# Performance work log

Measured on AMD Instinct MI355X. Metric: run time of the kernel, lower is better.

Reference implementation:

```python
import jax, jax.numpy as jnp
import numpy as np

B, QLEN, MLEN, E, H, DH = 2, 1024, 1024, 1024, 16, 64
KLEN = QLEN + MLEN
LN_EPS = 1e-3  # keras LayerNormalization default epsilon


def layer_norm(x, gamma, beta):
    mu = jnp.mean(x, axis=-1, keepdims=True)
    var = jnp.mean(jnp.square(x - mu), axis=-1, keepdims=True)
    return (x - mu) * jax.lax.rsqrt(var + LN_EPS) * gamma + beta


def rel_shift(x):
    # x: [B, H, q, k] -> standard Transformer-XL relative shift
    b, h, q, k = x.shape
    x = jnp.pad(x, ((0, 0), (0, 0), (0, 0), (1, 0)))
    x = x.reshape(b, h, k + 1, q)[:, :, 1:, :]
    return x.reshape(b, h, q, k)


def setup_inputs() -> dict:
    key = jax.random.key(0)
    ks = jax.random.split(key, 12)
    s = 0.02
    inp = {
        "w": jax.random.normal(ks[0], (B, QLEN, E), jnp.float32),
        "r": jax.random.normal(ks[1], (1, KLEN, E), jnp.float32),
        "member": jax.random.normal(ks[2], (B, MLEN, E), jnp.float32),
        # causal mask over concatenated keys: 1 = masked
        "attn_mask": (jnp.arange(KLEN)[None, :] > (jnp.arange(QLEN)[:, None] + MLEN)).astype(jnp.float32),
        "Wq": jax.random.normal(ks[3], (E, H * DH), jnp.float32) * s,
        "Wk": jax.random.normal(ks[4], (E, H * DH), jnp.float32) * s,
        "Wv": jax.random.normal(ks[5], (E, H * DH), jnp.float32) * s,
        "Wr": jax.random.normal(ks[6], (E, H * DH), jnp.float32) * s,
        "Wo": jax.random.normal(ks[7], (H * DH, E), jnp.float32) * s,
        "r_w_bias": jnp.zeros((H, DH), jnp.float32),
        "r_r_bias": jnp.zeros((H, DH), jnp.float32),
        "ln1_g": jnp.ones((E,), jnp.float32),
        "ln1_b": jnp.zeros((E,), jnp.float32),
        "W1": jax.random.normal(ks[8], (E, 4 * E), jnp.float32) * s,
        "W2": jax.random.normal(ks[9], (4 * E, E), jnp.float32) * s,
        "ln2_g": jnp.ones((E,), jnp.float32),
        "ln2_b": jnp.zeros((E,), jnp.float32),
    }
    return inp


def reference(w, r, member, attn_mask, Wq, Wk, Wv, Wr, Wo, r_w_bias, r_r_bias,
              ln1_g, ln1_b, W1, W2, ln2_g, ln2_b):
    b, qlen, e = w.shape
    h, dh = r_w_bias.shape
    cat = jnp.concatenate([member, w], axis=1)          # [B, klen, E]
    q = (cat @ Wq)[:, -qlen:]                           # [B, q, H*DH]
    k = cat @ Wk                                        # [B, klen, H*DH]
    v = cat @ Wv
    rp = (r @ Wr)[0]                                    # [klen, H*DH] (shared over batch)
    qh = q.reshape(b, qlen, h, dh)
    kh = k.reshape(b, -1, h, dh)
    vh = v.reshape(b, -1, h, dh)
    rh = rp.reshape(-1, h, dh)
    AC = jnp.einsum('bqhd,bkhd->bhqk', qh + r_w_bias, kh)
    BD = jnp.einsum('bqhd,khd->bhqk', qh + r_r_bias, rh)
    BD = rel_shift(BD)
    attn = (AC + BD) / jnp.sqrt(jnp.float32(e))         # note: scaled by sqrt(embed_size)
    m = attn_mask[None, None]                           # [1,1,q,klen]
    attn = attn * (1.0 - m) - 1e30 * m
    p = jax.nn.softmax(attn, axis=-1)
    o = jnp.einsum('bhqk,bkhd->bqhd', p, vh).reshape(b, qlen, h * dh)
    o = o @ Wo
    x = layer_norm(w + o, ln1_g, ln1_b)
    y = jax.nn.relu(x @ W1) @ W2
    return layer_norm(y + x, ln2_g, ln2_b)
```

## Files before the change

### kernel.cpp

```cpp
#include <hip/hip_runtime.h>
#include <hip/hip_bf16.h>
#include <stdint.h>

typedef __bf16 bf16x8 __attribute__((ext_vector_type(8)));
typedef float  f32x4  __attribute__((ext_vector_type(4)));

constexpr int BB   = 2;
constexpr int QL   = 1024;
constexpr int ML   = 1024;
constexpr int KL   = 2048;
constexpr int ED   = 1024;
constexpr int HH   = 16;
constexpr int FF   = 4096;
constexpr size_t MN = 2048u * 1024u;

__device__ __forceinline__ bf16x8 ld8(const __hip_bfloat16* p) {
    return *reinterpret_cast<const bf16x8*>(p);
}
__device__ __forceinline__ void st8(__hip_bfloat16* p, bf16x8 v) {
    *reinterpret_cast<bf16x8*>(p) = v;
}
__device__ __forceinline__ f32x4 mfma16(bf16x8 a, bf16x8 b, f32x4 c) {
    return __builtin_amdgcn_mfma_f32_16x16x32_bf16(a, b, c, 0, 0, 0);
}
__device__ __forceinline__ void async16(void* lds, const void* g) {
    __builtin_amdgcn_global_load_lds((__attribute__((address_space(1))) void*)g,
                                     (__attribute__((address_space(3))) void*)lds,
                                     16, 0, 0);
}

__global__ __launch_bounds__(256) void build_cat_r(const float* __restrict__ w,
                                                   const float* __restrict__ mem,
                                                   const float* __restrict__ r,
                                                   __hip_bfloat16* __restrict__ cat,
                                                   __hip_bfloat16* __restrict__ rbf) {
    const int bx = blockIdx.x;
    const float* src;
    __hip_bfloat16* dst;
    size_t g;
    if (bx < 2048) {
        size_t t = (size_t)bx * 256 + threadIdx.x;
        g = t * 8;
        int b   = (int)(g >> 21);
        int rem = (int)(g & ((1u << 21) - 1));
        int j = rem >> 10, e = rem & 1023;
        src = (j < ML) ? &mem[((size_t)b * ML + j) * ED + e]
                       : &w[((size_t)b * QL + (j - ML)) * ED + e];
        dst = &cat[g];
    } else {
        g = ((size_t)(bx - 2048) * 256 + threadIdx.x) * 8;
        src = &r[g];
        dst = &rbf[g];
    }
    float4 f0 = *(const float4*)src;
    float4 f1 = *(const float4*)(src + 4);
    union { bf16x8 v; __hip_bfloat16 h[8]; } u;
    u.h[0] = __float2bfloat16(f0.x); u.h[1] = __float2bfloat16(f0.y);
    u.h[2] = __float2bfloat16(f0.z); u.h[3] = __float2bfloat16(f0.w);
    u.h[4] = __float2bfloat16(f1.x); u.h[5] = __float2bfloat16(f1.y);
    u.h[6] = __float2bfloat16(f1.z); u.h[7] = __float2bfloat16(f1.w);
    st8(dst, u.v);
}

__global__ __launch_bounds__(256) void transpose_cast(const float* __restrict__ in,
                                                      __hip_bfloat16* __restrict__ out,
                                                      int K, int N) {
    __shared__ float tile[32][33];
    const int tx = threadIdx.x & 31, ty = threadIdx.x >> 5;
    const int n0 = blockIdx.x * 32, k0 = blockIdx.y * 32;
#pragma unroll
    for (int i = 0; i < 4; ++i)
        tile[ty + i * 8][tx] = in[(size_t)(k0 + ty + i * 8) * N + n0 + tx];
    __syncthreads();
#pragma unroll
    for (int i = 0; i < 4; ++i)
        out[(size_t)(n0 + ty + i * 8) * K + k0 + tx] = __float2bfloat16(tile[tx][ty + i * 8]);
}

__global__ __launch_bounds__(256) void tc5(const float* __restrict__ s0, const float* __restrict__ s1,
                                           const float* __restrict__ s2, const float* __restrict__ s3,
                                           const float* __restrict__ s4,
                                           __hip_bfloat16* __restrict__ wqkvT,
                                           __hip_bfloat16* __restrict__ wot) {
    __shared__ float tile[32][33];
    const int z = blockIdx.z;
    const float* in = (z == 0) ? s0 : (z == 1) ? s1 : (z == 2) ? s2 : (z == 3) ? s3 : s4;
    __hip_bfloat16* out = (z == 4) ? wot : wqkvT + (size_t)z * 1024 * 1024;
    const int tx = threadIdx.x & 31, ty = threadIdx.x >> 5;
    const int n0 = blockIdx.x * 32, k0 = blockIdx.y * 32;
#pragma unroll
    for (int i = 0; i < 4; ++i)
        tile[ty + i * 8][tx] = in[(size_t)(k0 + ty + i * 8) * 1024 + n0 + tx];
    __syncthreads();
#pragma unroll
    for (int i = 0; i < 4; ++i)
        out[(size_t)(n0 + ty + i * 8) * 1024 + k0 + tx] = __float2bfloat16(tile[tx][ty + i * 8]);
}

__global__ __launch_bounds__(256) void transpose_v(const __hip_bfloat16* __restrict__ v,
                                                   __hip_bfloat16* __restrict__ vt) {
    __shared__ __hip_bfloat16 tile[32][33];
    const int tx = threadIdx.x & 31, ty = threadIdx.x >> 5;
    const int s = blockIdx.z, b = s >> 4, h = s & 15;
    const int j0 = blockIdx.x * 32, d0 = blockIdx.y * 32;
#pragma unroll
    for (int i = 0; i < 4; ++i)
        tile[ty + i * 8][tx] =
            v[((size_t)b * KL + j0 + ty + i * 8) * 1024 + h * 64 + d0 + tx];
    __syncthreads();
#pragma unroll
    for (int i = 0; i < 4; ++i)
        vt[((size_t)s * 64 + d0 + ty + i * 8) * KL + j0 + tx] = tile[tx][ty + i * 8];
}

template <int EPI, bool SK>
__global__ __launch_bounds__(256) void gemm_bt(const __hip_bfloat16* __restrict__ A,
                                               const __hip_bfloat16* __restrict__ Bt,
                                               void* __restrict__ Cv,
                                               int N, int kLen, int lda, int ldb) {
    __shared__ __align__(16) __hip_bfloat16 sA[128 * 32];
    __shared__ __align__(16) __hip_bfloat16 sB[128 * 32];
    const int tid = threadIdx.x;
    const int lane = tid & 63;
    const int l16 = lane & 15, quad = lane >> 4;
    const int wv = tid >> 6;
    const int wm = wv >> 1, wn = wv & 1;
    const int bm = blockIdx.y * 128, bn = blockIdx.x * 128;
    const int kOff = SK ? blockIdx.z * kLen : 0;
    const int c0 = tid, c1 = 256 + tid;
    const int r0 = c0 >> 2, o0 = (c0 & 3) * 8;
    const int r1 = c1 >> 2, o1 = (c1 & 3) * 8;
    f32x4 acc[4][4] = {};
    for (int k0 = 0; k0 < kLen; k0 += 32) {
        async16(&sA[c0 * 8], A + (size_t)(bm + r0) * lda + kOff + k0 + o0);
        async16(&sA[c1 * 8], A + (size_t)(bm + r1) * lda + kOff + k0 + o1);
        async16(&sB[c0 * 8], Bt + (size_t)(bn + r0) * ldb + kOff + k0 + o0);
        async16(&sB[c1 * 8], Bt + (size_t)(bn + r1) * ldb + kOff + k0 + o1);
        __syncthreads();
        bf16x8 af[4], bfr[4];
#pragma unroll
        for (int i = 0; i < 4; ++i)
            af[i] = ld8(&sA[(wm * 64 + i * 16 + l16) * 32 + quad * 8]);
#pragma unroll
        for (int j = 0; j < 4; ++j)
            bfr[j] = ld8(&sB[(wn * 64 + j * 16 + l16) * 32 + quad * 8]);
#pragma unroll
        for (int i = 0; i < 4; ++i)
#pragma unroll
            for (int j = 0; j < 4; ++j)
                acc[i][j] = mfma16(af[i], bfr[j], acc[i][j]);
        __syncthreads();
    }
#pragma unroll
    for (int i = 0; i < 4; ++i)
#pragma unroll
        for (int j = 0; j < 4; ++j)
#pragma unroll
            for (int rg = 0; rg < 4; ++rg) {
                size_t row = bm + wm * 64 + i * 16 + quad * 4 + rg;
                size_t col = bn + wn * 64 + j * 16 + l16;
                float v = acc[i][j][rg];
                if (EPI == 0) {
                    float* C = (float*)Cv + (SK ? (size_t)blockIdx.z * MN : 0);
                    C[row * N + col] = v;
                } else {
                    __hip_bfloat16* C = (__hip_bfloat16*)Cv;
                    C[row * N + col] = __float2bfloat16(fmaxf(v, 0.f));
                }
            }
}

__global__ __launch_bounds__(256) void gemm_qkvr(const __hip_bfloat16* __restrict__ cat,
                                                 const __hip_bfloat16* __restrict__ rbf,
                                                 const __hip_bfloat16* __restrict__ Bt,
                                                 __hip_bfloat16* __restrict__ qwb,
                                                 __hip_bfloat16* __restrict__ qrb,
                                                 __hip_bfloat16* __restrict__ kbuf,
                                                 __hip_bfloat16* __restrict__ vbuf,
                                                 __hip_bfloat16* __restrict__ rpb,
                                                 const float* __restrict__ rwb,
                                                 const float* __restrict__ rrb) {
    const int bm = blockIdx.y * 128, bn = blockIdx.x * 128;
    const int region = blockIdx.x >> 3;
    if (region == 0 && (bm & 2047) < 1024) return;
    if (region == 3 && bm >= 2048) return;
    const __hip_bfloat16* A = (region == 3) ? rbf : cat;
    __shared__ __align__(16) __hip_bfloat16 sA[128 * 32];
    __shared__ __align__(16) __hip_bfloat16 sB[128 * 32];
    const int tid = threadIdx.x;
    const int lane = tid & 63;
    const int l16 = lane & 15, quad = lane >> 4;
    const int wv = tid >> 6;
    const int wm = wv >> 1, wn = wv & 1;
    const int c0 = tid, c1 = 256 + tid;
    const int r0 = c0 >> 2, o0 = (c0 & 3) * 8;
    const int r1 = c1 >> 2, o1 = (c1 & 3) * 8;
    f32x4 acc[4][4] = {};
    for (int k0 = 0; k0 < 1024; k0 += 32) {
        async16(&sA[c0 * 8], A + (size_t)(bm + r0) * 1024 + k0 + o0);
        async16(&sA[c1 * 8], A + (size_t)(bm + r1) * 1024 + k0 + o1);
        async16(&sB[c0 * 8], Bt + (size_t)(bn + r0) * 1024 + k0 + o0);
        async16(&sB[c1 * 8], Bt + (size_t)(bn + r1) * 1024 + k0 + o1);
        __syncthreads();
        bf16x8 af[4], bfr[4];
#pragma unroll
        for (int i = 0; i < 4; ++i)
            af[i] = ld8(&sA[(wm * 64 + i * 16 + l16) * 32 + quad * 8]);
#pragma unroll
        for (int j = 0; j < 4; ++j)
            bfr[j] = ld8(&sB[(wn * 64 + j * 16 + l16) * 32 + quad * 8]);
#pragma unroll
        for (int i = 0; i < 4; ++i)
#pragma unroll
            for (int j = 0; j < 4; ++j)
                acc[i][j] = mfma16(af[i], bfr[j], acc[i][j]);
        __syncthreads();
    }
#pragma unroll
    for (int j = 0; j < 4; ++j) {
        const int col = bn + wn * 64 + j * 16 + l16;
        float bw = 0.f, br = 0.f;
        if (region == 0) { bw = rwb[col]; br = rrb[col]; }
#pragma unroll
        for (int i = 0; i < 4; ++i)
#pragma unroll
            for (int rg = 0; rg < 4; ++rg) {
                const int row = bm + wm * 64 + i * 16 + quad * 4 + rg;
                const int bb = row >> 11, jr = row & 2047;
                float v = acc[i][j][rg];
                if (region == 0) {
                    size_t o = ((size_t)(bb * 1024 + (jr - 1024))) * 1024 + col;
                    qwb[o] = __float2bfloat16(v + bw);
                    qrb[o] = __float2bfloat16(v + br);
                } else if (region == 1) {
                    kbuf[((size_t)(bb * 2048 + jr)) * 1024 + (col - 1024)] = __float2bfloat16(v);
                } else if (region == 2) {
                    vbuf[((size_t)(bb * 2048 + jr)) * 1024 + (col - 2048)] = __float2bfloat16(v);
                } else {
                    rpb[(size_t)row * 1024 + (col - 3072)] = __float2bfloat16(v);
                }
            }
    }
}

__global__ __launch_bounds__(64, 3) void flash_attn3(
        const __hip_bfloat16* __restrict__ qw, const __hip_bfloat16* __restrict__ qr,
        const __hip_bfloat16* __restrict__ kbuf, const __hip_bfloat16* __restrict__ vtb,
        const __hip_bfloat16* __restrict__ rpb,
        float* __restrict__ Opart, float* __restrict__ lpart) {
    __shared__ __align__(16) __hip_bfloat16 spb[32][76];
    const int lane = threadIdx.x;
    const int l16 = lane & 15, quad = lane >> 4;
    const int qi = blockIdx.x >> 1, chunk = blockIdx.x & 1;
    const int h = blockIdx.y, b = blockIdx.z;
    const int i0 = qi * 32;

    bf16x8 qaw[2][2], qar[2][2];
#pragma unroll
    for (int g = 0; g < 2; ++g)
#pragma unroll
        for (int kf = 0; kf < 2; ++kf) {
            size_t qi_ = ((size_t)(b * QL + i0 + g * 16 + l16)) * 1024 + h * 64 + kf * 32 + quad * 8;
            qaw[g][kf] = ld8(&qw[qi_]);
            qar[g][kf] = ld8(&qr[qi_]);
        }
    f32x4 oacc[2][4] = {};
    f32x4 lacc[2] = {};
    union { bf16x8 v; __hip_bfloat16 h8[8]; } ou;
#pragma unroll
    for (int j = 0; j < 8; ++j) ou.h8[j] = __float2bfloat16(l16 == 0 ? 1.f : 0.f);
    const bf16x8 onesf = ou.v;

    int srcIdx[4], selr[4];
#pragma unroll
    for (int r = 0; r < 4; ++r) {
        int s = l16 + 15 - (quad * 4 + r);
        selr[r] = s >> 4;
        srcIdx[r] = (quad * 16) | (s & 15);
    }
    const int T = (i0 + 1119) >> 6, Ta = T >> 1;
    const int t0 = chunk ? Ta : 0, t1 = chunk ? T : Ta;
    const __hip_bfloat16* kB = kbuf + (size_t)b * KL * 1024 + h * 64;
    const __hip_bfloat16* vB = vtb + ((size_t)(b * HH + h) * 64) * 2048;
    const __hip_bfloat16* rB = rpb + h * 64;

    for (int jt = t0; jt < t1; ++jt) {
        const int j0 = jt * 64;
        f32x4 sfr[2][4];
#pragma unroll
        for (int nt = 0; nt < 4; ++nt) {
            const __hip_bfloat16* kr = kB + (size_t)(j0 + nt * 16 + l16) * 1024 + quad * 8;
            bf16x8 b0 = ld8(kr);
            bf16x8 b1 = ld8(kr + 32);
#pragma unroll
            for (int g = 0; g < 2; ++g) {
                f32x4 z = {};
                z = mfma16(qaw[g][0], b0, z);
                z = mfma16(qaw[g][1], b1, z);
                sfr[g][nt] = z;
            }
        }
        f32x4 bd[2][5];
        const int ubase = j0 - i0 + 992;
#pragma unroll
        for (int s = 0; s < 6; ++s) {
            int row = ubase + s * 16 + l16;
            if (row > 2047) row = 2047;
            const __hip_bfloat16* rr = rB + (size_t)row * 1024 + quad * 8;
            bf16x8 f0 = ld8(rr);
            bf16x8 f1 = ld8(rr + 32);
            if (s >= 1) {
                f32x4 z = {};
                z = mfma16(qar[0][0], f0, z);
                z = mfma16(qar[0][1], f1, z);
                bd[0][s - 1] = z;
            }
            if (s <= 4) {
                f32x4 z = {};
                z = mfma16(qar[1][0], f0, z);
                z = mfma16(qar[1][1], f1, z);
                bd[1][s] = z;
            }
        }
#pragma unroll
        for (int g = 0; g < 2; ++g) {
            float pre[5][4];
#pragma unroll
            for (int t = 0; t < 5; ++t)
#pragma unroll
                for (int r = 0; r < 4; ++r)
                    pre[t][r] = __shfl(bd[g][t][r], srcIdx[r], 64);
#pragma unroll
            for (int nt = 0; nt < 4; ++nt)
#pragma unroll
                for (int r = 0; r < 4; ++r) {
                    float bdv = selr[r] ? pre[nt + 1][r] : pre[nt][r];
                    float sv = (sfr[g][nt][r] + bdv) * 0.03125f;
                    int ii = i0 + g * 16 + quad * 4 + r;
                    int jj = j0 + nt * 16 + l16;
                    float p = (jj <= ii + ML) ? __expf(sv) : 0.f;
                    spb[g * 16 + quad * 4 + r][nt * 16 + l16] = __float2bfloat16(p);
                }
        }
        bf16x8 pa[2][2];
#pragma unroll
        for (int g = 0; g < 2; ++g) {
            pa[g][0] = ld8(&spb[g * 16 + l16][quad * 8]);
            pa[g][1] = ld8(&spb[g * 16 + l16][32 + quad * 8]);
            lacc[g] = mfma16(pa[g][0], onesf, lacc[g]);
            lacc[g] = mfma16(pa[g][1], onesf, lacc[g]);
        }
#pragma unroll
        for (int dt = 0; dt < 4; ++dt) {
            const __hip_bfloat16* vr = vB + (size_t)(dt * 16 + l16) * 2048 + j0 + quad * 8;
            bf16x8 v0 = ld8(vr);
            bf16x8 v1 = ld8(vr + 32);
#pragma unroll
            for (int g = 0; g < 2; ++g) {
                oacc[g][dt] = mfma16(pa[g][0], v0, oacc[g][dt]);
                oacc[g][dt] = mfma16(pa[g][1], v1, oacc[g][dt]);
            }
        }
    }
    const size_t obase = ((size_t)((chunk * 2 + b) * HH + h)) * (1024 * 64);
#pragma unroll
    for (int g = 0; g < 2; ++g)
#pragma unroll
        for (int dt = 0; dt < 4; ++dt)
#pragma unroll
            for (int r = 0; r < 4; ++r) {
                int q = i0 + g * 16 + quad * 4 + r;
                Opart[obase + (size_t)q * 64 + dt * 16 + l16] = oacc[g][dt][r];
            }
    if (l16 == 0) {
        const size_t lbase = ((size_t)((chunk * 2 + b) * HH + h)) * 1024;
#pragma unroll
        for (int g = 0; g < 2; ++g)
#pragma unroll
            for (int r = 0; r < 4; ++r) {
                int q = i0 + g * 16 + quad * 4 + r;
                lpart[lbase + q] = lacc[g][r];
            }
    }
}

__global__ __launch_bounds__(256) void combine_attn(const float* __restrict__ Opart,
                                                    const float* __restrict__ lpart,
                                                    __hip_bfloat16* __restrict__ og) {
    size_t t = (size_t)blockIdx.x * 256 + threadIdx.x;
    size_t e4 = t * 4;
    int d  = (int)(e4 & 63);
    int q  = (int)((e4 >> 6) & 1023);
    int hh = (int)((e4 >> 16) & 15);
    int bb = (int)(e4 >> 20);
    size_t i0 = ((size_t)(bb * HH + hh) * 1024 + q) * 64 + d;
    const size_t CS = (size_t)2 * HH * 1024 * 64;
    float4 o0 = *(const float4*)&Opart[i0];
    float4 o1 = *(const float4*)&Opart[i0 + CS];
    float l0 = lpart[(size_t)(bb * HH + hh) * 1024 + q];
    float l1 = lpart[(size_t)(bb * HH + hh) * 1024 + q + 2 * HH * 1024];
    float inv = 1.f / (l0 + l1);
    union { __hip_bfloat16 h[4]; uint2 u; } o;
    o.h[0] = __float2bfloat16((o0.x + o1.x) * inv);
    o.h[1] = __float2bfloat16((o0.y + o1.y) * inv);
    o.h[2] = __float2bfloat16((o0.z + o1.z) * inv);
    o.h[3] = __float2bfloat16((o0.w + o1.w) * inv);
    *(uint2*)&og[((size_t)bb * 1024 + q) * 1024 + hh * 64 + d] = o.u;
}

template <int NP, bool WB>
__global__ __launch_bounds__(256) void add_ln_k(const float* __restrict__ res,
                                                const float* __restrict__ parts,
                                                const float* __restrict__ gam,
                                                const float* __restrict__ bet,
                                                float* __restrict__ of,
                                                __hip_bfloat16* __restrict__ ob) {
    const int tid = threadIdx.x;
    const size_t base = (size_t)blockIdx.x * ED;
    const int col = tid * 4;
    float4 va = *(const float4*)&res[base + col];
    float x0 = va.x, x1 = va.y, x2 = va.z, x3 = va.w;
#pragma unroll
    for (int z = 0; z < NP; ++z) {
        float4 p = *(const float4*)&parts[(size_t)z * MN + base + col];
        x0 += p.x; x1 += p.y; x2 += p.z; x3 += p.w;
    }
    float s1 = x0 + x1 + x2 + x3;
    float s2 = x0 * x0 + x1 * x1 + x2 * x2 + x3 * x3;
    for (int o = 32; o > 0; o >>= 1) {
        s1 += __shfl_down(s1, o, 64);
        s2 += __shfl_down(s2, o, 64);
    }
    __shared__ float p1[4], p2[4];
    if ((tid & 63) == 0) { p1[tid >> 6] = s1; p2[tid >> 6] = s2; }
    __syncthreads();
    float S1 = p1[0] + p1[1] + p1[2] + p1[3];
    float S2 = p2[0] + p2[1] + p2[2] + p2[3];
    float mu = S1 * (1.0f / ED);
    float var = S2 * (1.0f / ED) - mu * mu;
    float rs = rsqrtf(var + 1e-3f);
    float4 g4 = *(const float4*)&gam[col];
    float4 b4 = *(const float4*)&bet[col];
    float y0 = (x0 - mu) * rs * g4.x + b4.x;
    float y1 = (x1 - mu) * rs * g4.y + b4.y;
    float y2 = (x2 - mu) * rs * g4.z + b4.z;
    float y3 = (x3 - mu) * rs * g4.w + b4.w;
    *(float4*)&of[base + col] = make_float4(y0, y1, y2, y3);
    if (WB) {
        ob[base + col + 0] = __float2bfloat16(y0);
        ob[base + col + 1] = __float2bfloat16(y1);
        ob[base + col + 2] = __float2bfloat16(y2);
        ob[base + col + 3] = __float2bfloat16(y3);
    }
}

extern "C" void kernel_launch(void* const* d_in, const int* in_sizes, int n_in,
                              void* d_out, int out_size, void* d_ws, size_t ws_size,
                              hipStream_t stream) {
    const float* w   = (const float*)d_in[0];
    const float* r   = (const float*)d_in[1];
    const float* mem = (const float*)d_in[2];
    const float* Wq  = (const float*)d_in[4];
    const float* Wk  = (const float*)d_in[5];
    const float* Wv  = (const float*)d_in[6];
    const float* Wr  = (const float*)d_in[7];
    const float* Wo  = (const float*)d_in[8];
    const float* rwb = (const float*)d_in[9];
    const float* rrb = (const float*)d_in[10];
    const float* g1  = (const float*)d_in[11];
    const float* b1  = (const float*)d_in[12];
    const float* W1  = (const float*)d_in[13];
    const float* W2  = (const float*)d_in[14];
    const float* g2  = (const float*)d_in[15];
    const float* b2  = (const float*)d_in[16];

    char* ws = (char*)d_ws;
    size_t off = 0;
    auto alloc = [&](size_t bytes) -> void* {
        void* p = ws + off;
        off += (bytes + 255) & ~(size_t)255;
        return p;
    };
    __hip_bfloat16* wqkvT = (__hip_bfloat16*)alloc((size_t)4096 * 1024 * 2);
    __hip_bfloat16* wot   = (__hip_bfloat16*)alloc((size_t)ED * ED * 2);
    __hip_bfloat16* w1t   = (__hip_bfloat16*)alloc((size_t)FF * ED * 2);
    __hip_bfloat16* w2t   = (__hip_bfloat16*)alloc((size_t)ED * FF * 2);
    __hip_bfloat16* qwb   = (__hip_bfloat16*)alloc((size_t)BB * QL * ED * 2);
    __hip_bfloat16* qrb   = (__hip_bfloat16*)alloc((size_t)BB * QL * ED * 2);
    __hip_bfloat16* vtb   = (__hip_bfloat16*)alloc((size_t)BB * KL * ED * 2);
    __hip_bfloat16* rpb   = (__hip_bfloat16*)alloc((size_t)KL * ED * 2);
    __hip_bfloat16* og    = (__hip_bfloat16*)alloc((size_t)BB * QL * ED * 2);
    char* regA = (char*)alloc((size_t)BB * KL * ED * 2);
    __hip_bfloat16* cat = (__hip_bfloat16*)regA;
    float*          xf  = (float*)regA;
    char* regB = (char*)alloc((size_t)KL * ED * 2);
    __hip_bfloat16* rbf = (__hip_bfloat16*)regB;
    __hip_bfloat16* xb  = (__hip_bfloat16*)regB;
    char* regC = (char*)alloc((size_t)BB * QL * FF * 2);
    __hip_bfloat16* kbuf = (__hip_bfloat16*)regC;
    __hip_bfloat16* vbuf = (__hip_bfloat16*)(regC + (size_t)BB * KL * ED * 2);
    __hip_bfloat16* y1   = (__hip_bfloat16*)regC;
    char* regE = (char*)alloc((size_t)4 * MN * 4);
    float* Opart  = (float*)regE;
    float* lpart  = (float*)(regE + (size_t)2 * BB * HH * QL * 64 * 4);
    float* o_part = (float*)regE;
    float* f_part = (float*)regE;
    if (off > ws_size) return;

    build_cat_r<<<3072, 256, 0, stream>>>(w, mem, r, cat, rbf);
    tc5<<<dim3(32, 32, 5), 256, 0, stream>>>(Wq, Wk, Wv, Wr, Wo, wqkvT, wot);
    transpose_cast<<<dim3(128, 32), 256, 0, stream>>>(W1, w1t, 1024, 4096);
    transpose_cast<<<dim3(32, 128), 256, 0, stream>>>(W2, w2t, 4096, 1024);

    gemm_qkvr<<<dim3(32, 32), 256, 0, stream>>>(cat, rbf, wqkvT, qwb, qrb, kbuf, vbuf, rpb,
                                                rwb, rrb);
    transpose_v<<<dim3(64, 2, 32), 256, 0, stream>>>(vbuf, vtb);

    flash_attn3<<<dim3(64, 16, 2), 64, 0, stream>>>(qwb, qrb, kbuf, vtb, rpb, Opart, lpart);
    combine_attn<<<2048, 256, 0, stream>>>(Opart, lpart, og);

    gemm_bt<0, true><<<dim3(8, 16, 4), 256, 0, stream>>>(og, wot, o_part, 1024, 256, 1024, 1024);
    add_ln_k<4, true><<<2048, 256, 0, stream>>>(w, o_part, g1, b1, xf, xb);

    gemm_bt<2, false><<<dim3(32, 16, 1), 256, 0, stream>>>(xb, w1t, y1, 4096, 1024, 1024, 1024);
    gemm_bt<0, true><<<dim3(8, 16, 4), 256, 0, stream>>>(y1, w2t, f_part, 1024, 1024, 4096, 4096);
    add_ln_k<4, false><<<2048, 256, 0, stream>>>(xf, f_part, g2, b2, (float*)d_out, nullptr);
}
```

Measured before the change: 443.6 us.

## Split attention keys into four chunks and remap blocks for XCD-local head grouping

The flash attention kernel now splits each query tile's key range into four chunks instead of two and launches a flat 4096-block grid. Block IDs are decoded so that blocks on the same XCD (id & 7) share a batch-head pair, which is meant to improve L2 reuse of K/V/R. The combine kernel now sums four partial outputs and normalizers. This adds more partial-output traffic and a larger workspace in exchange for more parallelism and better cache locality; launch bounds also move to 4 waves per SIMD.

```diff
diff --git a/kernel.cpp b/kernel.cpp
--- a/kernel.cpp
+++ b/kernel.cpp
@@ -243,7 +243,7 @@
     }
 }
 
-__global__ __launch_bounds__(64, 3) void flash_attn3(
+__global__ __launch_bounds__(64, 4) void flash_attn4(
         const __hip_bfloat16* __restrict__ qw, const __hip_bfloat16* __restrict__ qr,
         const __hip_bfloat16* __restrict__ kbuf, const __hip_bfloat16* __restrict__ vtb,
         const __hip_bfloat16* __restrict__ rpb,
@@ -251,8 +251,14 @@
     __shared__ __align__(16) __hip_bfloat16 spb[32][76];
     const int lane = threadIdx.x;
     const int l16 = lane & 15, quad = lane >> 4;
-    const int qi = blockIdx.x >> 1, chunk = blockIdx.x & 1;
-    const int h = blockIdx.y, b = blockIdx.z;
+    const int id    = blockIdx.x;
+    const int xcd   = id & 7;
+    const int rest  = id >> 3;
+    const int grp   = rest >> 7;
+    const int local = rest & 127;
+    const int p     = grp * 8 + xcd;
+    const int b = p >> 4, h = p & 15;
+    const int qi = local >> 2, chunk = local & 3;
     const int i0 = qi * 32;
 
     bf16x8 qaw[2][2], qar[2][2];
@@ -278,8 +284,8 @@
         selr[r] = s >> 4;
         srcIdx[r] = (quad * 16) | (s & 15);
     }
-    const int T = (i0 + 1119) >> 6, Ta = T >> 1;
-    const int t0 = chunk ? Ta : 0, t1 = chunk ? T : Ta;
+    const int T = (i0 + 1119) >> 6;
+    const int t0 = (chunk * T) >> 2, t1 = ((chunk + 1) * T) >> 2;
     const __hip_bfloat16* kB = kbuf + (size_t)b * KL * 1024 + h * 64;
     const __hip_bfloat16* vB = vtb + ((size_t)(b * HH + h) * 64) * 2048;
     const __hip_bfloat16* rB = rpb + h * 64;
@@ -338,8 +344,8 @@
                     float sv = (sfr[g][nt][r] + bdv) * 0.03125f;
                     int ii = i0 + g * 16 + quad * 4 + r;
                     int jj = j0 + nt * 16 + l16;
-                    float p = (jj <= ii + ML) ? __expf(sv) : 0.f;
-                    spb[g * 16 + quad * 4 + r][nt * 16 + l16] = __float2bfloat16(p);
+                    float p_ = (jj <= ii + ML) ? __expf(sv) : 0.f;
+                    spb[g * 16 + quad * 4 + r][nt * 16 + l16] = __float2bfloat16(p_);
                 }
         }
         bf16x8 pa[2][2];
@@ -393,18 +399,20 @@
     int q  = (int)((e4 >> 6) & 1023);
     int hh = (int)((e4 >> 16) & 15);
     int bb = (int)(e4 >> 20);
-    size_t i0 = ((size_t)(bb * HH + hh) * 1024 + q) * 64 + d;
-    const size_t CS = (size_t)2 * HH * 1024 * 64;
-    float4 o0 = *(const float4*)&Opart[i0];
-    float4 o1 = *(const float4*)&Opart[i0 + CS];
-    float l0 = lpart[(size_t)(bb * HH + hh) * 1024 + q];
-    float l1 = lpart[(size_t)(bb * HH + hh) * 1024 + q + 2 * HH * 1024];
-    float inv = 1.f / (l0 + l1);
+    float ox = 0.f, oy = 0.f, oz = 0.f, ow = 0.f, l = 0.f;
+#pragma unroll
+    for (int c = 0; c < 4; ++c) {
+        size_t gsel = (size_t)((c * 2 + bb) * HH + hh);
+        float4 o = *(const float4*)&Opart[gsel * (1024 * 64) + (size_t)q * 64 + d];
+        ox += o.x; oy += o.y; oz += o.z; ow += o.w;
+        l += lpart[gsel * 1024 + q];
+    }
+    float inv = 1.f / l;
     union { __hip_bfloat16 h[4]; uint2 u; } o;
-    o.h[0] = __float2bfloat16((o0.x + o1.x) * inv);
-    o.h[1] = __float2bfloat16((o0.y + o1.y) * inv);
-    o.h[2] = __float2bfloat16((o0.z + o1.z) * inv);
-    o.h[3] = __float2bfloat16((o0.w + o1.w) * inv);
+    o.h[0] = __float2bfloat16(ox * inv);
+    o.h[1] = __float2bfloat16(oy * inv);
+    o.h[2] = __float2bfloat16(oz * inv);
+    o.h[3] = __float2bfloat16(ow * inv);
     *(uint2*)&og[((size_t)bb * 1024 + q) * 1024 + hh * 64 + d] = o.u;
 }
 
@@ -500,9 +508,13 @@
     __hip_bfloat16* kbuf = (__hip_bfloat16*)regC;
     __hip_bfloat16* vbuf = (__hip_bfloat16*)(regC + (size_t)BB * KL * ED * 2);
     __hip_bfloat16* y1   = (__hip_bfloat16*)regC;
-    char* regE = (char*)alloc((size_t)4 * MN * 4);
+    const size_t opartBytes = (size_t)8 * HH * QL * 64 * 4;
+    const size_t lpartBytes = (size_t)8 * HH * QL * 4;
+    size_t regEsz = opartBytes + lpartBytes;
+    if (regEsz < (size_t)4 * MN * 4) regEsz = (size_t)4 * MN * 4;
+    char* regE = (char*)alloc(regEsz);
     float* Opart  = (float*)regE;
-    float* lpart  = (float*)(regE + (size_t)2 * BB * HH * QL * 64 * 4);
+    float* lpart  = (float*)(regE + opartBytes);
     float* o_part = (float*)regE;
     float* f_part = (float*)regE;
     if (off > ws_size) return;
@@ -516,7 +528,7 @@
                                                 rwb, rrb);
     transpose_v<<<dim3(64, 2, 32), 256, 0, stream>>>(vbuf, vtb);
 
-    flash_attn3<<<dim3(64, 16, 2), 64, 0, stream>>>(qwb, qrb, kbuf, vtb, rpb, Opart, lpart);
+    flash_attn4<<<dim3(4096), 64, 0, stream>>>(qwb, qrb, kbuf, vtb, rpb, Opart, lpart);
     combine_attn<<<2048, 256, 0, stream>>>(Opart, lpart, og);
 
     gemm_bt<0, true><<<dim3(8, 16, 4), 256, 0, stream>>>(og, wot, o_part, 1024, 256, 1024, 1024);
```

Result: slower. 490.4 us (+10.6%).
